# Kernel tuning notes

Hardware: AMD Instinct MI355X
Metric: run time of the kernel (lower is better)

Reference implementation:

```python
import jax, jax.numpy as jnp
import numpy as np

B, C, H, W = 4, 256, 128, 128
K = 3
BN = max(16, C // 4)  # 64
PAD = K // 2
EPS = 1e-5


def conv2d(x, w, b=None, pad=0):
    out = jax.lax.conv_general_dilated(
        x, w, (1, 1), [(pad, pad), (pad, pad)],
        dimension_numbers=("NCHW", "OIHW", "NCHW"))
    if b is not None:
        out = out + b[None, :, None, None]
    return out


def deform_conv2d(z, offset, mask, w, b):
    # torchvision modulated deform conv v2: offset [B,2*K*K,H,W] interleaved (dy,dx),
    # mask [B,K*K,H,W], kernel positions row-major, stride 1, pad PAD.
    Bz, Cb, Hz, Wz = z.shape
    K2 = K * K
    off = offset.reshape(Bz, K2, 2, Hz, Wz)
    ky, kx = jnp.meshgrid(jnp.arange(K), jnp.arange(K), indexing="ij")
    # sampling positions py/px: [B, K2, H, W]
    py = off[:, :, 0] + jnp.arange(Hz)[None, None, :, None] + (ky.reshape(K2) - PAD)[None, :, None, None]
    px = off[:, :, 1] + jnp.arange(Wz)[None, None, None, :] + (kx.reshape(K2) - PAD)[None, :, None, None]
    y0 = jnp.floor(py)
    x0 = jnp.floor(px)
    wy1 = py - y0  # frac weights
    wx1 = px - x0
    z_flat = z.reshape(Bz, Cb, Hz * Wz)

    def gather(yy, xx, wgt):
        valid = (yy >= 0) & (yy < Hz) & (xx >= 0) & (xx < Wz)
        yc = jnp.clip(yy, 0, Hz - 1).astype(jnp.int32)
        xc = jnp.clip(xx, 0, Wz - 1).astype(jnp.int32)
        idx = (yc * Wz + xc).reshape(Bz, K2 * Hz * Wz)
        g = jnp.take_along_axis(z_flat, idx[:, None, :], axis=2)  # [B, Cb, K2*H*W]
        g = g.reshape(Bz, Cb, K2, Hz, Wz)
        return g * (wgt * valid.astype(z.dtype))[:, None]

    val = (gather(y0, x0, (1 - wy1) * (1 - wx1))
           + gather(y0, x0 + 1, (1 - wy1) * wx1)
           + gather(y0 + 1, x0, wy1 * (1 - wx1))
           + gather(y0 + 1, x0 + 1, wy1 * wx1))
    val = val * mask[:, None]  # modulate: [B, Cb, K2, H, W]
    out = jnp.einsum("bckhw,ock->bohw", val, w.reshape(w.shape[0], Cb, K2))
    return out + b[None, :, None, None]


def setup_inputs() -> dict:
    key = jax.random.key(0)
    ks = jax.random.split(key, 11)
    s = 0.05
    return {
        "x": jax.random.normal(ks[0], (B, C, H, W), jnp.float32),
        "down_w": jax.random.normal(ks[1], (BN, C, 1, 1), jnp.float32) * s,
        "off_w": jax.random.normal(ks[2], (2 * K * K, BN, 3, 3), jnp.float32) * s,
        "off_b": jax.random.normal(ks[3], (2 * K * K,), jnp.float32) * s,
        "mask_w": jax.random.normal(ks[4], (K * K, BN, 3, 3), jnp.float32) * s,
        "mask_b": jax.random.normal(ks[5], (K * K,), jnp.float32) * s,
        "def_w": jax.random.normal(ks[6], (BN, BN, K, K), jnp.float32) * s,
        "def_b": jax.random.normal(ks[7], (BN,), jnp.float32) * s,
        "up_w": jax.random.normal(ks[8], (C, BN, 1, 1), jnp.float32) * s,
        "gamma": jnp.ones((C,), jnp.float32),
        "beta": jnp.zeros((C,), jnp.float32),
    }


def reference(x, down_w, off_w, off_b, mask_w, mask_b, def_w, def_b, up_w, gamma, beta):
    z = conv2d(x, down_w)                               # 1x1 down: [B, BN, H, W]
    offset = conv2d(z, off_w, off_b, pad=1)             # [B, 18, H, W]
    mask = jax.nn.sigmoid(conv2d(z, mask_w, mask_b, pad=1))  # [B, 9, H, W]
    z = deform_conv2d(z, offset, mask, def_w, def_b)    # [B, BN, H, W]
    z = conv2d(z, up_w)                                 # 1x1 up: [B, C, H, W]
    y = x + z
    # BatchNorm2d in training mode: batch statistics over (B, H, W), biased var
    mean = jnp.mean(y, axis=(0, 2, 3), keepdims=True)
    var = jnp.var(y, axis=(0, 2, 3), keepdims=True)
    yh = (y - mean) * jax.lax.rsqrt(var + EPS)
    yh = yh * gamma[None, :, None, None] + beta[None, :, None, None]
    return yh * jax.nn.sigmoid(yh)  # SiLU
```

## Files before the change

### kernel.cpp

```cpp
#include <hip/hip_runtime.h>
#include <hip/hip_bf16.h>


typedef __attribute__((ext_vector_type(8))) short bf16x8;
typedef __attribute__((ext_vector_type(4))) float f32x4;

#define HW   16384
#define CC   256
#define BNC  64

#define WS_STATS   0
#define WS_SS      131072
#define WS_FD      135168
#define WS_FOM     167936
#define WS_FDEF    204800
#define WS_FUP     278528
#define WS_ZBF     311296
#define WS_OM      8699904
#define WS_Z2      15777792

__device__ __forceinline__ short f2b(float f) {
    unsigned u = __float_as_uint(f);
    unsigned r = (u + 0x7FFFu + ((u >> 16) & 1u)) >> 16;
    return (short)r;
}
__device__ __forceinline__ float b2f(short s) {
    return __uint_as_float(((unsigned)(unsigned short)s) << 16);
}

__global__ void k_prep(const float* __restrict__ down_w, const float* __restrict__ off_w,
                       const float* __restrict__ mask_w, const float* __restrict__ def_w,
                       const float* __restrict__ up_w, char* __restrict__ ws) {
    int g = blockIdx.x * 256 + threadIdx.x;
    int row = g >> 6, lane = g & 63;
    if (row >= 172) return;
    int l15 = lane & 15, q = lane >> 4;
    short vals[8];
    short* dst;
    if (row < 32) {
        int nt = row >> 3, kk = row & 7;
        int n = nt * 16 + l15;
        for (int j = 0; j < 8; ++j) {
            int c = kk * 32 + q * 8 + j;
            vals[j] = f2b(down_w[n * 256 + c]);
        }
        dst = (short*)(ws + WS_FD) + row * 512 + lane * 8;
    } else if (row < 68) {
        int r = row - 32; int nt = r / 18, kk = r % 18;
        int n = nt * 16 + l15;
        for (int j = 0; j < 8; ++j) {
            int kap = kk * 32 + q * 8 + j; int k = kap >> 6, c = kap & 63;
            float v = 0.f;
            if (n < 18)      v = off_w[(n * 64 + c) * 9 + k];
            else if (n < 27) v = mask_w[((n - 18) * 64 + c) * 9 + k];
            vals[j] = f2b(v);
        }
        dst = (short*)(ws + WS_FOM) + r * 512 + lane * 8;
    } else if (row < 140) {
        int r = row - 68; int nt = r / 18, kk = r % 18;
        int n = nt * 16 + l15;
        for (int j = 0; j < 8; ++j) {
            int kap = kk * 32 + q * 8 + j; int k = kap >> 6, c = kap & 63;
            vals[j] = f2b(def_w[(n * 64 + c) * 9 + k]);
        }
        dst = (short*)(ws + WS_FDEF) + r * 512 + lane * 8;
    } else {
        int r = row - 140; int nt = r >> 1, kk = r & 1;
        int o = nt * 16 + l15;
        for (int j = 0; j < 8; ++j) {
            int c = kk * 32 + q * 8 + j;
            vals[j] = f2b(up_w[o * 64 + c]);
        }
        dst = (short*)(ws + WS_FUP) + r * 512 + lane * 8;
    }
    for (int j = 0; j < 8; ++j) dst[j] = vals[j];
}

__global__ __launch_bounds__(256) void k_down(const float* __restrict__ x,
                                              const short* __restrict__ wfd,
                                              short* __restrict__ zbf) {
    __shared__ __align__(16) short xl[64 * 264];
    int blk = blockIdx.x;
    int b = blk >> 8;
    int hw0 = (blk & 255) * 64;
    int t = threadIdx.x;
    const float* xb = x + (size_t)b * CC * HW + hw0;
    int px = t & 63, w = t >> 6;
    for (int i = 0; i < 64; ++i) {
        int c = w + i * 4;
        xl[px * 264 + c] = f2b(xb[(size_t)c * HW + px]);
    }
    __syncthreads();
    int lane = t & 63, wv = t >> 6;
    int l15 = lane & 15, q = lane >> 4;
    bf16x8 A[8];
    const short* xrow = &xl[(wv * 16 + l15) * 264];
    for (int kk = 0; kk < 8; ++kk)
        A[kk] = *(const bf16x8*)(xrow + kk * 32 + q * 8);
    const bf16x8* Bp = (const bf16x8*)wfd;
    size_t obase = ((size_t)b * HW + hw0 + wv * 16) * 64;
    for (int nt = 0; nt < 4; ++nt) {
        f32x4 acc = {0.f, 0.f, 0.f, 0.f};
        for (int kk = 0; kk < 8; ++kk) {
            bf16x8 Bf = Bp[(nt * 8 + kk) * 64 + lane];
            acc = __builtin_amdgcn_mfma_f32_16x16x32_bf16(A[kk], Bf, acc, 0, 0, 0);
        }
        int n = nt * 16 + l15;
        for (int r = 0; r < 4; ++r) {
            int prow = q * 4 + r;
            zbf[obase + (size_t)prow * 64 + n] = f2b(acc[r]);
        }
    }
}

__global__ __launch_bounds__(256) void k_offmask(const short* __restrict__ zbf,
                                                 const short* __restrict__ wfom,
                                                 const float* __restrict__ off_b,
                                                 const float* __restrict__ mask_b,
                                                 float* __restrict__ om) {
    int blk = blockIdx.x;
    int b = blk >> 8;
    int hw0 = (blk & 255) * 64;
    int y = hw0 >> 7, x0 = hw0 & 127;
    int t = threadIdx.x, lane = t & 63, wv = t >> 6;
    int l15 = lane & 15, q = lane >> 4;
    int xx0 = x0 + wv * 16 + l15;
    const short* zb = zbf + (size_t)b * HW * 64;
    f32x4 acc0 = {0, 0, 0, 0}, acc1 = {0, 0, 0, 0};
    const bf16x8* Bp = (const bf16x8*)wfom;
    for (int kk = 0; kk < 18; ++kk) {
        int k = kk >> 1;
        int yy = y + (k / 3) - 1;
        int xx = xx0 + (k % 3) - 1;
        int c0 = (kk & 1) * 32 + q * 8;
        bf16x8 A = {0, 0, 0, 0, 0, 0, 0, 0};
        if (yy >= 0 && yy < 128 && xx >= 0 && xx < 128)
            A = *(const bf16x8*)(zb + ((size_t)(yy * 128 + xx)) * 64 + c0);
        bf16x8 B0 = Bp[kk * 64 + lane];
        bf16x8 B1 = Bp[(18 + kk) * 64 + lane];
        acc0 = __builtin_amdgcn_mfma_f32_16x16x32_bf16(A, B0, acc0, 0, 0, 0);
        acc1 = __builtin_amdgcn_mfma_f32_16x16x32_bf16(A, B1, acc1, 0, 0, 0);
    }
    float* omb = om + ((size_t)b * HW + hw0 + wv * 16) * 27;
    for (int half = 0; half < 2; ++half) {
        f32x4 acc = half ? acc1 : acc0;
        int n = half * 16 + l15;
        if (n < 27) {
            for (int r = 0; r < 4; ++r) {
                int prow = q * 4 + r;
                float v = acc[r];
                if (n < 18) v += off_b[n];
                else { v += mask_b[n - 18]; v = 1.f / (1.f + __expf(-v)); }
                omb[prow * 27 + n] = v;
            }
        }
    }
}

__global__ __launch_bounds__(256) void k_deform(const short* __restrict__ zbf,
                                                const float* __restrict__ om,
                                                const short* __restrict__ wfdef,
                                                const float* __restrict__ def_b,
                                                short* __restrict__ z2) {
    __shared__ int   pAi[144 * 4];
    __shared__ float pAw[144 * 4];
    __shared__ __align__(16) short valA[18 * 64 * 8];
    int blk = blockIdx.x;
    int b = blk >> 10;
    int hw0 = (blk & 1023) * 16;
    int y = hw0 >> 7, x0 = hw0 & 127;
    int t = threadIdx.x;
    if (t < 144) {
        int px = t / 9, k = t % 9;
        const float* p = om + ((size_t)b * HW + hw0 + px) * 27;
        float dy = p[2 * k], dx = p[2 * k + 1], m = p[18 + k];
        float py  = (float)y + (float)(k / 3 - 1) + dy;
        float pxf = (float)(x0 + px) + (float)(k % 3 - 1) + dx;
        float fy = floorf(py), fx = floorf(pxf);
        int iy = (int)fy, ix = (int)fx;
        float wy = py - fy, wx = pxf - fx;
        float ww[4] = { (1.f - wy) * (1.f - wx) * m, (1.f - wy) * wx * m,
                        wy * (1.f - wx) * m,          wy * wx * m };
        int ys[2] = {iy, iy + 1}, xs[2] = {ix, ix + 1};
        for (int ci = 0; ci < 4; ++ci) {
            int cy = ys[ci >> 1], cx = xs[ci & 1];
            bool v = (cy >= 0 && cy < 128 && cx >= 0 && cx < 128);
            pAi[t * 4 + ci] = v ? (cy * 128 + cx) * 64 : 0;
            pAw[t * 4 + ci] = v ? ww[ci] : 0.f;
        }
    }
    __syncthreads();
    int lane = t & 63, wv = t >> 6;
    const unsigned short* zb = (const unsigned short*)zbf + (size_t)b * HW * 64;
    for (int it = 0; it < 36; ++it) {
        int task = wv * 36 + it;
        int px = task / 9, k = task % 9;
        int c = lane;
        float val = 0.f;
        for (int ci = 0; ci < 4; ++ci)
            val += pAw[task * 4 + ci] * b2f((short)zb[pAi[task * 4 + ci] + c]);
        int elem = ((k * 2 + (c >> 5)) * 64 + px + 16 * ((c >> 3) & 3)) * 8 + (c & 7);
        valA[elem] = f2b(val);
    }
    __syncthreads();
    int l15 = lane & 15, q = lane >> 4;
    f32x4 acc = {0, 0, 0, 0};
    const bf16x8* Bp = (const bf16x8*)wfdef;
    const bf16x8* Ap = (const bf16x8*)valA;
    for (int kk = 0; kk < 18; ++kk) {
        bf16x8 A  = Ap[kk * 64 + lane];
        bf16x8 Bf = Bp[(wv * 18 + kk) * 64 + lane];
        acc = __builtin_amdgcn_mfma_f32_16x16x32_bf16(A, Bf, acc, 0, 0, 0);
    }
    int n = wv * 16 + l15;
    float bias = def_b[n];
    short* z2b = z2 + ((size_t)b * HW + hw0) * 64;
    for (int r = 0; r < 4; ++r) {
        int prow = q * 4 + r;
        z2b[prow * 64 + n] = f2b(acc[r] + bias);
    }
}

__global__ __launch_bounds__(256) void k_up(const short* __restrict__ z2,
                                            const short* __restrict__ wfup,
                                            const float* __restrict__ x,
                                            float* __restrict__ yout,
                                            float* __restrict__ stats) {
    __shared__ float yl[16 * 257];
    int blk = blockIdx.x;
    int b = blk >> 10;
    int hw0 = (blk & 1023) * 16;
    int t = threadIdx.x, lane = t & 63, wv = t >> 6;
    int l15 = lane & 15, q = lane >> 4;
    const short* z2b = z2 + ((size_t)b * HW + hw0) * 64;
    bf16x8 A0 = *(const bf16x8*)(z2b + (size_t)l15 * 64 + q * 8);
    bf16x8 A1 = *(const bf16x8*)(z2b + (size_t)l15 * 64 + 32 + q * 8);
    const bf16x8* Bp = (const bf16x8*)wfup;
    for (int ntl = 0; ntl < 4; ++ntl) {
        int nt = wv * 4 + ntl;
        f32x4 acc = {0, 0, 0, 0};
        acc = __builtin_amdgcn_mfma_f32_16x16x32_bf16(A0, Bp[(nt * 2 + 0) * 64 + lane], acc, 0, 0, 0);
        acc = __builtin_amdgcn_mfma_f32_16x16x32_bf16(A1, Bp[(nt * 2 + 1) * 64 + lane], acc, 0, 0, 0);
        int o = nt * 16 + l15;
        for (int r = 0; r < 4; ++r) yl[(q * 4 + r) * 257 + o] = acc[r];
    }
    __syncthreads();
    int px = t & 15, og = t >> 4;
    int bucket = blk & 63;
    const float* xb = x + (size_t)b * CC * HW + hw0 + px;
    float* yb = yout + (size_t)b * CC * HW + hw0 + px;
    for (int i = 0; i < 16; ++i) {
        int o = og + i * 16;
        float v = yl[px * 257 + o] + xb[(size_t)o * HW];
        yb[(size_t)o * HW] = v;
        float s = v, s2 = v * v;
        for (int m = 8; m >= 1; m >>= 1) { s += __shfl_xor(s, m); s2 += __shfl_xor(s2, m); }
        if (px == 0) {
            atomicAdd(&stats[bucket * 512 + o], s);
            atomicAdd(&stats[bucket * 512 + 256 + o], s2);
        }
    }
}

__global__ void k_stats(const float* __restrict__ stats, const float* __restrict__ gamma,
                        const float* __restrict__ beta, float* __restrict__ ss) {
    int o = threadIdx.x;
    float s = 0.f, s2 = 0.f;
    for (int u = 0; u < 64; ++u) { s += stats[u * 512 + o]; s2 += stats[u * 512 + 256 + o]; }
    float mean = s * (1.f / 65536.f);
    float var  = s2 * (1.f / 65536.f) - mean * mean;
    float rs = rsqrtf(var + 1e-5f);
    float sc = gamma[o] * rs;
    ss[o]       = sc;
    ss[256 + o] = beta[o] - mean * sc;
}

__global__ __launch_bounds__(256) void k_bn(float* __restrict__ y, const float* __restrict__ ss) {
    int g = blockIdx.x * 256 + threadIdx.x;
    int o = (g >> 10) & 255;
    float sc = ss[o], sh = ss[256 + o];
    float4* p = (float4*)y + (size_t)g * 4;
    for (int i = 0; i < 4; ++i) {
        float4 v = p[i];
        float* f = (float*)&v;
        for (int j = 0; j < 4; ++j) {
            float h = f[j] * sc + sh;
            f[j] = h / (1.f + __expf(-h));
        }
        p[i] = v;
    }
}

extern "C" void kernel_launch(void* const* d_in, const int* in_sizes, int n_in,
                              void* d_out, int out_size, void* d_ws, size_t ws_size,
                              hipStream_t stream) {
    const float* x      = (const float*)d_in[0];
    const float* down_w = (const float*)d_in[1];
    const float* off_w  = (const float*)d_in[2];
    const float* off_b  = (const float*)d_in[3];
    const float* mask_w = (const float*)d_in[4];
    const float* mask_b = (const float*)d_in[5];
    const float* def_w  = (const float*)d_in[6];
    const float* def_b  = (const float*)d_in[7];
    const float* up_w   = (const float*)d_in[8];
    const float* gamma  = (const float*)d_in[9];
    const float* beta   = (const float*)d_in[10];
    char* ws = (char*)d_ws;
    float* stats = (float*)(ws + WS_STATS);
    float* ss    = (float*)(ws + WS_SS);
    short* wfd   = (short*)(ws + WS_FD);
    short* wfom  = (short*)(ws + WS_FOM);
    short* wfdef = (short*)(ws + WS_FDEF);
    short* wfup  = (short*)(ws + WS_FUP);
    short* zbf   = (short*)(ws + WS_ZBF);
    float* om    = (float*)(ws + WS_OM);
    short* z2    = (short*)(ws + WS_Z2);
    float* y     = (float*)d_out;

    hipMemsetAsync(stats, 0, 64 * 512 * sizeof(float), stream);
    hipLaunchKernelGGL(k_prep,    dim3(43),   dim3(256), 0, stream, down_w, off_w, mask_w, def_w, up_w, ws);
    hipLaunchKernelGGL(k_down,    dim3(1024), dim3(256), 0, stream, x, wfd, zbf);
    hipLaunchKernelGGL(k_offmask, dim3(1024), dim3(256), 0, stream, zbf, wfom, off_b, mask_b, om);
    hipLaunchKernelGGL(k_deform,  dim3(4096), dim3(256), 0, stream, zbf, om, wfdef, def_b, z2);
    hipLaunchKernelGGL(k_up,      dim3(4096), dim3(256), 0, stream, z2, wfup, x, y, stats);
    hipLaunchKernelGGL(k_stats,   dim3(1),    dim3(256), 0, stream, stats, gamma, beta, ss);
    hipLaunchKernelGGL(k_bn,      dim3(4096), dim3(256), 0, stream, y, ss);
}
```

Before: 284.5 us.

## Vectorize deform gather, LDS packing, and up-proj epilogue with fewer atomics

The deformable gather now has each thread load 8 channels at once (a 16-byte vector load) per bilinear corner, instead of one bf16 per lane. The repacked deform weight fragment layout matches the new valA order. The down kernel writes packed bf16x8 into LDS. The up-projection epilogue now assigns one output channel per thread, using float4 loads and stores of x and y and one atomic pair per channel instead of shuffle reductions. These changes cut scalar memory transactions and atomics, at the cost of likely LDS bank conflicts in the strided yl reads and per-row strided global accesses.

Measured after the change: 271.9 us. -4.4%, faster.

```diff
diff --git a/kernel.cpp b/kernel.cpp
--- a/kernel.cpp
+++ b/kernel.cpp
@@ -59,8 +59,9 @@
     } else if (row < 140) {
         int r = row - 68; int nt = r / 18, kk = r % 18;
         int n = nt * 16 + l15;
+        int u = kk * 4 + q, k = u >> 3;
         for (int j = 0; j < 8; ++j) {
-            int kap = kk * 32 + q * 8 + j; int k = kap >> 6, c = kap & 63;
+            int c = (u & 7) * 8 + j;
             vals[j] = f2b(def_w[(n * 64 + c) * 9 + k]);
         }
         dst = (short*)(ws + WS_FDEF) + r * 512 + lane * 8;
@@ -86,9 +87,13 @@
     int t = threadIdx.x;
     const float* xb = x + (size_t)b * CC * HW + hw0;
     int px = t & 63, w = t >> 6;
-    for (int i = 0; i < 64; ++i) {
-        int c = w + i * 4;
-        xl[px * 264 + c] = f2b(xb[(size_t)c * HW + px]);
+    for (int h = 0; h < 8; ++h) {
+        int c0 = h * 32 + w * 8;
+        bf16x8 pk;
+        #pragma unroll
+        for (int j = 0; j < 8; ++j)
+            pk[j] = f2b(xb[(size_t)(c0 + j) * HW + px]);
+        *(bf16x8*)(&xl[px * 264 + c0]) = pk;
     }
     __syncthreads();
     int lane = t & 63, wv = t >> 6;
@@ -162,8 +167,8 @@
                                                 const short* __restrict__ wfdef,
                                                 const float* __restrict__ def_b,
                                                 short* __restrict__ z2) {
-    __shared__ int   pAi[144 * 4];
-    __shared__ float pAw[144 * 4];
+    __shared__ int4   pAi4[144];
+    __shared__ float4 pAw4[144];
     __shared__ __align__(16) short valA[18 * 64 * 8];
     int blk = blockIdx.x;
     int b = blk >> 10;
@@ -182,27 +187,47 @@
         float ww[4] = { (1.f - wy) * (1.f - wx) * m, (1.f - wy) * wx * m,
                         wy * (1.f - wx) * m,          wy * wx * m };
         int ys[2] = {iy, iy + 1}, xs[2] = {ix, ix + 1};
+        int   ri[4]; float rw[4];
         for (int ci = 0; ci < 4; ++ci) {
             int cy = ys[ci >> 1], cx = xs[ci & 1];
             bool v = (cy >= 0 && cy < 128 && cx >= 0 && cx < 128);
-            pAi[t * 4 + ci] = v ? (cy * 128 + cx) * 64 : 0;
-            pAw[t * 4 + ci] = v ? ww[ci] : 0.f;
-        }
+            ri[ci] = v ? (cy * 128 + cx) * 64 : 0;
+            rw[ci] = v ? ww[ci] : 0.f;
+        }
+        pAi4[t] = make_int4(ri[0], ri[1], ri[2], ri[3]);
+        pAw4[t] = make_float4(rw[0], rw[1], rw[2], rw[3]);
+    }
+    __syncthreads();
+    const unsigned short* zb = (const unsigned short*)zbf + (size_t)b * HW * 64;
+    for (int s = t; s < 1152; s += 256) {
+        int px = s & 15, u = s >> 4;
+        int k = u >> 3, cg = u & 7;
+        int task = px * 9 + k;
+        int4   idx = pAi4[task];
+        float4 wt  = pAw4[task];
+        int   ii[4] = { idx.x, idx.y, idx.z, idx.w };
+        float wwt[4] = { wt.x, wt.y, wt.z, wt.w };
+        float acc[8] = {0.f, 0.f, 0.f, 0.f, 0.f, 0.f, 0.f, 0.f};
+        #pragma unroll
+        for (int ci = 0; ci < 4; ++ci) {
+            float w = wwt[ci];
+            int4 d = *(const int4*)(zb + ii[ci] + cg * 8);
+            int dp[4] = { d.x, d.y, d.z, d.w };
+            #pragma unroll
+            for (int p = 0; p < 4; ++p) {
+                float lo = __uint_as_float((unsigned)dp[p] << 16);
+                float hi = __uint_as_float((unsigned)dp[p] & 0xffff0000u);
+                acc[2 * p]     += w * lo;
+                acc[2 * p + 1] += w * hi;
+            }
+        }
+        bf16x8 out;
+        #pragma unroll
+        for (int j = 0; j < 8; ++j) out[j] = f2b(acc[j]);
+        *(bf16x8*)(&valA[s * 8]) = out;
     }
     __syncthreads();
     int lane = t & 63, wv = t >> 6;
-    const unsigned short* zb = (const unsigned short*)zbf + (size_t)b * HW * 64;
-    for (int it = 0; it < 36; ++it) {
-        int task = wv * 36 + it;
-        int px = task / 9, k = task % 9;
-        int c = lane;
-        float val = 0.f;
-        for (int ci = 0; ci < 4; ++ci)
-            val += pAw[task * 4 + ci] * b2f((short)zb[pAi[task * 4 + ci] + c]);
-        int elem = ((k * 2 + (c >> 5)) * 64 + px + 16 * ((c >> 3) & 3)) * 8 + (c & 7);
-        valA[elem] = f2b(val);
-    }
-    __syncthreads();
     int l15 = lane & 15, q = lane >> 4;
     f32x4 acc = {0, 0, 0, 0};
     const bf16x8* Bp = (const bf16x8*)wfdef;
@@ -245,21 +270,28 @@
         for (int r = 0; r < 4; ++r) yl[(q * 4 + r) * 257 + o] = acc[r];
     }
     __syncthreads();
-    int px = t & 15, og = t >> 4;
+    int o = t;
+    size_t pbase = (size_t)b * CC * HW + (size_t)o * HW + hw0;
+    const float4* xv = (const float4*)(x + pbase);
+    float4* yv = (float4*)(yout + pbase);
+    float s = 0.f, s2 = 0.f;
+    #pragma unroll
+    for (int g4 = 0; g4 < 4; ++g4) {
+        float4 xvv = xv[g4];
+        float xf[4] = { xvv.x, xvv.y, xvv.z, xvv.w };
+        float of[4];
+        #pragma unroll
+        for (int j = 0; j < 4; ++j) {
+            int px = g4 * 4 + j;
+            float v = yl[px * 257 + o] + xf[j];
+            of[j] = v;
+            s += v; s2 += v * v;
+        }
+        yv[g4] = make_float4(of[0], of[1], of[2], of[3]);
+    }
     int bucket = blk & 63;
-    const float* xb = x + (size_t)b * CC * HW + hw0 + px;
-    float* yb = yout + (size_t)b * CC * HW + hw0 + px;
-    for (int i = 0; i < 16; ++i) {
-        int o = og + i * 16;
-        float v = yl[px * 257 + o] + xb[(size_t)o * HW];
-        yb[(size_t)o * HW] = v;
-        float s = v, s2 = v * v;
-        for (int m = 8; m >= 1; m >>= 1) { s += __shfl_xor(s, m); s2 += __shfl_xor(s2, m); }
-        if (px == 0) {
-            atomicAdd(&stats[bucket * 512 + o], s);
-            atomicAdd(&stats[bucket * 512 + 256 + o], s2);
-        }
-    }
+    atomicAdd(&stats[bucket * 512 + o], s);
+    atomicAdd(&stats[bucket * 512 + 256 + o], s2);
 }
 
 __global__ void k_stats(const float* __restrict__ stats, const float* __restrict__ gamma,
@@ -282,12 +314,12 @@
     float4* p = (float4*)y + (size_t)g * 4;
     for (int i = 0; i < 4; ++i) {
         float4 v = p[i];
-        float* f = (float*)&v;
+        float vf[4] = { v.x, v.y, v.z, v.w };
         for (int j = 0; j < 4; ++j) {
-            float h = f[j] * sc + sh;
-            f[j] = h / (1.f + __expf(-h));
-        }
-        p[i] = v;
+            float h = vf[j] * sc + sh;
+            vf[j] = h / (1.f + __expf(-h));
+        }
+        p[i] = make_float4(vf[0], vf[1], vf[2], vf[3]);
     }
 }
 
```
